# Kernel optimization log

Hardware: AMD Instinct MI355X
Metric: run time of the kernel (lower is better)

## Reference

```python
import jax, jax.numpy as jnp
import numpy as np

LN_EPS = 1e-5

def _layer_norm(x, g, b):
    mu = jnp.mean(x, axis=-1, keepdims=True)
    var = jnp.mean(jnp.square(x - mu), axis=-1, keepdims=True)
    return g * (x - mu) * jax.lax.rsqrt(var + LN_EPS) + b

def setup_inputs() -> dict:
    key = jax.random.key(0)
    ks = jax.random.split(key, 12)
    N, E, D, V = 25000, 400000, 128, 16
    x = jax.random.normal(ks[0], (N, 3), dtype=jnp.float32)
    h = jax.random.normal(ks[1], (N, D), dtype=jnp.float32)
    edge_index = jax.random.randint(ks[2], (2, E), 0, N, dtype=jnp.int64)
    local_frames = jax.random.normal(ks[3], (N, 3, 3), dtype=jnp.float32)
    batch = jnp.zeros((N,), dtype=jnp.int64)
    v_prev = jax.random.normal(ks[4], (N, V, 3), dtype=jnp.float32)
    # vector_init params: Linear(D, 3V) -> LN -> SiLU -> Linear(3V, 3V) -> LN -> SiLU
    lim1 = np.sqrt(6.0 / (D + 3 * V))
    W1 = jax.random.uniform(ks[5], (3 * V, D), minval=-lim1, maxval=lim1, dtype=jnp.float32)
    b1 = jnp.zeros((3 * V,), jnp.float32)
    g1 = jnp.ones((3 * V,), jnp.float32); bb1 = jnp.zeros((3 * V,), jnp.float32)
    lim2 = np.sqrt(6.0 / (3 * V + 3 * V))
    W2 = jax.random.uniform(ks[6], (3 * V, 3 * V), minval=-lim2, maxval=lim2, dtype=jnp.float32)
    b2 = jnp.zeros((3 * V,), jnp.float32)
    g2 = jnp.ones((3 * V,), jnp.float32); bb2 = jnp.zeros((3 * V,), jnp.float32)
    # vector_interaction params: Linear(2D, 2V*V) -> LN -> Sigmoid
    limi = np.sqrt(6.0 / (2 * D + 2 * V * V))
    Wi = jax.random.uniform(ks[7], (2 * V * V, 2 * D), minval=-limi, maxval=limi, dtype=jnp.float32)
    bi = jnp.zeros((2 * V * V,), jnp.float32)
    gi = jnp.ones((2 * V * V,), jnp.float32); bbi = jnp.zeros((2 * V * V,), jnp.float32)
    return {"x": x, "h": h, "edge_index": edge_index, "local_frames": local_frames,
            "batch": batch, "v_prev": v_prev,
            "W1": W1, "b1": b1, "g1": g1, "bb1": bb1,
            "W2": W2, "b2": b2, "g2": g2, "bb2": bb2,
            "Wi": Wi, "bi": bi, "gi": gi, "bbi": bbi}

def reference(x, h, edge_index, local_frames, batch, v_prev,
              W1, b1, g1, bb1, W2, b2, g2, bb2, Wi, bi, gi, bbi):
    N = x.shape[0]
    V = v_prev.shape[1]  # vector_dim
    row, col = edge_index[0], edge_index[1]
    # vector_init: two Linear+LN+SiLU blocks -> [N, V, 3]
    t = jax.nn.silu(_layer_norm(h @ W1.T + b1, g1, bb1))
    t = jax.nn.silu(_layer_norm(t @ W2.T + b2, g2, bb2))
    vectors = t.reshape(N, V, 3)
    hi, hj = h[col], h[row]           # [E, D]
    vi, vj = vectors[col], vectors[row]  # [E, V, 3]
    Ri, Rj = local_frames[col], local_frames[row]  # [E, 3, 3]
    # R_rel = Ri^T @ Rj
    R_rel = jnp.einsum('eji,ejk->eik', Ri, Rj)
    vj_in_i = jnp.einsum('eij,ecj->eci', R_rel, vj)  # rotate sender vectors
    stacked_vectors = jnp.concatenate([vi, vj_in_i], axis=1)  # [E, 2V, 3]
    stacked_norms = jnp.concatenate([hi, hj], axis=-1)        # [E, 2D]
    w = jax.nn.sigmoid(_layer_norm(stacked_norms @ Wi.T + bi, gi, bbi))
    int_weights = w.reshape(-1, 2 * V, V)                     # [E, 2V, V]
    v_new = jnp.einsum('eko,ekc->eco', stacked_vectors, int_weights)  # [E, V, 3]
    v_out = jax.ops.segment_sum(v_new, col, num_segments=N)  # scatter-add on receiver
    return v_prev + v_out
```

## Files before the change

kernel.cpp:

```cpp
#include <hip/hip_runtime.h>


#define DD 128
#define VV 16
#define TV 48
#define NK 512
#define LOG2E 1.44269504088896340736f

typedef __attribute__((ext_vector_type(8))) short short8;
typedef __attribute__((ext_vector_type(4))) float f32x4;

#if __has_builtin(__builtin_amdgcn_exp2f)
#define EXP2F(x) __builtin_amdgcn_exp2f(x)
#else
#define EXP2F(x) exp2f(x)
#endif
#if __has_builtin(__builtin_amdgcn_rcpf)
#define RCPF(x) __builtin_amdgcn_rcpf(x)
#else
#define RCPF(x) (1.0f/(x))
#endif

__device__ __forceinline__ unsigned short f2bf(float f){
    union{float f; unsigned u;} v; v.f = f;
    unsigned r = v.u + 0x7fffu + ((v.u >> 16) & 1u);
    return (unsigned short)(r >> 16);
}
__device__ __forceinline__ float bf2f(unsigned short h){
    union{unsigned u; float f;} v; v.u = ((unsigned)h) << 16; return v.f;
}
__device__ __forceinline__ float bf2f_hi(unsigned u){
    union{unsigned u; float f;} v; v.u = u & 0xffff0000u; return v.f;
}
__device__ __forceinline__ float bf2f_lo(unsigned u){
    union{unsigned u; float f;} v; v.u = u << 16; return v.f;
}
__device__ __forceinline__ void unpack8(uint4 q, float* d){
    d[0]=bf2f_lo(q.x); d[1]=bf2f_hi(q.x);
    d[2]=bf2f_lo(q.y); d[3]=bf2f_hi(q.y);
    d[4]=bf2f_lo(q.z); d[5]=bf2f_hi(q.z);
    d[6]=bf2f_lo(q.w); d[7]=bf2f_hi(q.w);
}
__device__ __forceinline__ float waveRedSum64(float v){
    #pragma unroll
    for (int off = 32; off > 0; off >>= 1) v += __shfl_xor(v, off, 64);
    return v;
}

__global__ void prep_k(const int* __restrict__ p, int nchk, int* __restrict__ flag,
                       int* __restrict__ cnt, int N){
    int i = blockIdx.x*blockDim.x + threadIdx.x;
    if (i < N) cnt[i] = 0;
    if (blockIdx.x == 0){
        __shared__ int s;
        if (threadIdx.x == 0) s = 0;
        __syncthreads();
        int nz = 0;
        for (int k = threadIdx.x; k < nchk; k += blockDim.x) nz |= (p[2*k+1] != 0);
        if (nz) atomicOr(&s, 1);
        __syncthreads();
        if (threadIdx.x == 0) *flag = s ? 0 : 1;
    }
}

__global__ void cvt_hist(const void* __restrict__ src, int* __restrict__ dst,
                         int* __restrict__ cnt, int n, int E,
                         const int* __restrict__ flag){
    int i = blockIdx.x*blockDim.x + threadIdx.x;
    if (i >= n) return;
    int v = (*flag) ? (int)((const long long*)src)[i] : ((const int*)src)[i];
    dst[i] = v;
    if (i >= E) atomicAdd(&cnt[v], 1);
}

__global__ __launch_bounds__(1024) void scan_k(const int* __restrict__ cnt,
        int* __restrict__ start, int* __restrict__ cursor, int N){
    __shared__ int wsum[16];
    __shared__ int woff[16];
    __shared__ int btot;
    __shared__ int carry;
    int tid = threadIdx.x;
    int lane = tid & 63, wid = tid >> 6;
    if (tid == 0) carry = 0;
    __syncthreads();
    for (int base = 0; base < N; base += 1024){
        int i = base + tid;
        int x = (i < N) ? cnt[i] : 0;
        int v = x;
        #pragma unroll
        for (int off = 1; off < 64; off <<= 1){
            int t = __shfl_up(v, off, 64);
            if (lane >= off) v += t;
        }
        if (lane == 63) wsum[wid] = v;
        __syncthreads();
        if (wid == 0 && lane < 16){
            int s = wsum[lane];
            int sv = s;
            #pragma unroll
            for (int off = 1; off < 16; off <<= 1){
                int t = __shfl_up(sv, off, 64);
                if (lane >= off) sv += t;
            }
            woff[lane] = sv - s;
            if (lane == 15) btot = sv;
        }
        __syncthreads();
        if (i < N){
            int excl = v - x + woff[wid] + carry;
            start[i] = excl;
            cursor[i] = excl;
        }
        __syncthreads();
        if (tid == 0) carry += btot;
        __syncthreads();
    }
    if (tid == 0) start[N] = carry;
}

__global__ void scatter_k(const int* __restrict__ idx, int* __restrict__ cursor,
                          int* __restrict__ elist, int E){
    int e = blockIdx.x*blockDim.x + threadIdx.x;
    if (e >= E) return;
    int col = idx[E + e], row = idx[e];
    int pos = atomicAdd(&cursor[col], 1);
    elist[pos] = row;
}

__global__ void build_wt(const float* __restrict__ Wi, const float* __restrict__ bi,
                         const float* __restrict__ gi, const float* __restrict__ bbi,
                         unsigned short* __restrict__ Wtb, float* __restrict__ bias_t,
                         float* __restrict__ gi_t, float* __restrict__ bbi_t){
    int j = blockIdx.x;
    int d = threadIdx.x;
    int half = j >> 9;
    int jj = j & 511;
    int c = jj >> 5, kk = jj & 31;
    int k = kk*16 + c;
    Wtb[(size_t)j*128 + d] = f2bf(Wi[k*256 + half*128 + d]);
    if (d == 0){
        bias_t[j] = half ? 0.0f : bi[k];
        if (!half){ gi_t[jj] = -gi[k]*LOG2E; bbi_t[jj] = -bbi[k]*LOG2E; }
    }
}

__global__ __launch_bounds__(256) void vinit(
        const float* __restrict__ h,
        const float* __restrict__ W1, const float* __restrict__ b1,
        const float* __restrict__ g1, const float* __restrict__ bb1,
        const float* __restrict__ W2, const float* __restrict__ b2,
        const float* __restrict__ g2, const float* __restrict__ bb2,
        const float* __restrict__ frames,
        float* __restrict__ vecs, float* __restrict__ gvec,
        unsigned short* __restrict__ hbh, unsigned short* __restrict__ hbl, int N){
    __shared__ float hs[4][DD];
    __shared__ float ts[4][TV];
    int w = threadIdx.x >> 6, l = threadIdx.x & 63;
    int n = blockIdx.x*4 + w;
    int nr = n < N ? n : N-1;
    float hv0 = h[(size_t)nr*DD + l];
    float hv1 = h[(size_t)nr*DD + 64 + l];
    hs[w][l]      = hv0;
    hs[w][l + 64] = hv1;
    if (n < N){
        unsigned short h0 = f2bf(hv0), h1 = f2bf(hv1);
        hbh[(size_t)n*DD + l]      = h0;
        hbh[(size_t)n*DD + 64 + l] = h1;
        hbl[(size_t)n*DD + l]      = f2bf(hv0 - bf2f(h0));
        hbl[(size_t)n*DD + 64 + l] = f2bf(hv1 - bf2f(h1));
    }
    __syncthreads();

    float o1 = 0.0f;
    if (l < TV){
        o1 = b1[l];
        const float* wr = W1 + l*DD;
        #pragma unroll
        for (int d = 0; d < DD; d += 4){
            float4 w4 = *(const float4*)(wr + d);
            o1 += hs[w][d]*w4.x + hs[w][d+1]*w4.y + hs[w][d+2]*w4.z + hs[w][d+3]*w4.w;
        }
    }
    float s  = waveRedSum64(l < TV ? o1 : 0.0f);
    float mu = s * (1.0f/TV);
    float dv = l < TV ? (o1 - mu) : 0.0f;
    float sq = waveRedSum64(dv*dv);
    float inv = rsqrtf(sq*(1.0f/TV) + 1e-5f);
    if (l < TV){
        float y = g1[l]*(dv*inv) + bb1[l];
        ts[w][l] = y / (1.0f + __expf(-y));
    }
    __syncthreads();

    float o2 = 0.0f;
    if (l < TV){
        o2 = b2[l];
        const float* wr = W2 + l*TV;
        #pragma unroll
        for (int j = 0; j < TV; j += 4){
            float4 w4 = *(const float4*)(wr + j);
            o2 += ts[w][j]*w4.x + ts[w][j+1]*w4.y + ts[w][j+2]*w4.z + ts[w][j+3]*w4.w;
        }
    }
    s  = waveRedSum64(l < TV ? o2 : 0.0f);
    mu = s * (1.0f/TV);
    dv = l < TV ? (o2 - mu) : 0.0f;
    sq = waveRedSum64(dv*dv);
    inv = rsqrtf(sq*(1.0f/TV) + 1e-5f);
    __syncthreads();
    if (l < TV){
        float y = g2[l]*(dv*inv) + bb2[l];
        float t2 = y / (1.0f + __expf(-y));
        if (n < N) vecs[(size_t)n*TV + l] = t2;
        ts[w][l] = t2;
    }
    __syncthreads();
    if (l < TV && n < N){
        int cc = l/3, oo = l%3;
        const float* R = frames + (size_t)n*9;
        float gv = R[oo*3+0]*ts[w][cc*3+0] + R[oo*3+1]*ts[w][cc*3+1] + R[oo*3+2]*ts[w][cc*3+2];
        gvec[(size_t)n*TV + l] = gv;
    }
}

__global__ __launch_bounds__(256) void gemm_mfma(
        const unsigned short* __restrict__ hbh, const unsigned short* __restrict__ hbl,
        const unsigned short* __restrict__ Wtb, const float* __restrict__ bias_t,
        unsigned short* __restrict__ P, int Np){
    int wv = threadIdx.x >> 6, l = threadIdx.x & 63;
    int lr = l & 15, g = l >> 4;
    int m0 = (blockIdx.y*4 + wv)*16;
    int n0 = blockIdx.x*256;

    f32x4 acc[16];
    #pragma unroll
    for (int nf = 0; nf < 16; nf++) acc[nf] = (f32x4){0.f,0.f,0.f,0.f};

    const unsigned short* arow_h = hbh + (size_t)(m0 + lr)*128;
    const unsigned short* arow_l = hbl + (size_t)(m0 + lr)*128;

    #pragma unroll
    for (int ks = 0; ks < 128; ks += 32){
        int kb = ks + 4*g;
        short8 ah, al;
        ((ushort4*)&ah)[0] = *(const ushort4*)(arow_h + kb);
        ((ushort4*)&ah)[1] = *(const ushort4*)(arow_h + kb + 16);
        ((ushort4*)&al)[0] = *(const ushort4*)(arow_l + kb);
        ((ushort4*)&al)[1] = *(const ushort4*)(arow_l + kb + 16);
        #pragma unroll
        for (int nf = 0; nf < 16; nf++){
            const unsigned short* brow = Wtb + (size_t)(n0 + nf*16 + lr)*128;
            short8 b;
            ((ushort4*)&b)[0] = *(const ushort4*)(brow + kb);
            ((ushort4*)&b)[1] = *(const ushort4*)(brow + kb + 16);
            acc[nf] = __builtin_amdgcn_mfma_f32_16x16x32_bf16(ah, b, acc[nf], 0, 0, 0);
            acc[nf] = __builtin_amdgcn_mfma_f32_16x16x32_bf16(al, b, acc[nf], 0, 0, 0);
        }
    }
    #pragma unroll
    for (int nf = 0; nf < 16; nf++){
        int col = n0 + nf*16 + lr;
        float bs = bias_t[col];
        #pragma unroll
        for (int r = 0; r < 4; r++){
            P[(size_t)(m0 + g*4 + r)*1024 + col] = f2bf(acc[nf][r] + bs);
        }
    }
}

__global__ __launch_bounds__(256) void node_k(
        const unsigned short* __restrict__ P, const float* __restrict__ vecs,
        const float* __restrict__ gvec, const float* __restrict__ frames,
        const int* __restrict__ start, const int* __restrict__ elist,
        const float* __restrict__ vprev, const float* __restrict__ gi_t,
        const float* __restrict__ bbi_t, float* __restrict__ out, int N){
    __shared__ float svs[4][4][100];
    int wv = threadIdx.x >> 6, ln = threadIdx.x & 63;
    int sub = ln >> 4, c = ln & 15;
    int n0 = blockIdx.x*4 + wv;
    int n = n0 < N ? n0 : N-1;

    {
        const float* vc = vecs + (size_t)n*TV + c*3;
        svs[wv][sub][c*3+0] = vc[0];
        svs[wv][sub][c*3+1] = vc[1];
        svs[wv][sub][c*3+2] = vc[2];
    }
    float R[9];
    #pragma unroll
    for (int i = 0; i < 9; i++) R[i] = frames[(size_t)n*9 + i];

    float pa[32];
    {
        const uint4* p4 = (const uint4*)(P + (size_t)n*1024 + c*32);
        #pragma unroll
        for (int q = 0; q < 4; q++) unpack8(p4[q], pa + 8*q);
    }
    int e0 = start[n], e1 = start[n+1];
    float a0 = 0.f, a1 = 0.f, a2 = 0.f;

    int t = e0 + sub;
    int rcur = elist[t < e1 ? t : 0];
    uint4 pb0, pb1, pb2, pb3;
    float gv0, gv1, gv2;
    {
        const uint4* p4 = (const uint4*)(P + (size_t)rcur*1024 + 512 + c*32);
        pb0 = p4[0]; pb1 = p4[1]; pb2 = p4[2]; pb3 = p4[3];
        const float* gr = gvec + (size_t)rcur*TV + c*3;
        gv0 = gr[0]; gv1 = gr[1]; gv2 = gr[2];
    }

    for (; t < e1; t += 4){
        int tn = t + 4;
        int rnext = elist[tn < e1 ? tn : 0];
        uint4 nb0, nb1, nb2, nb3;
        float ng0, ng1, ng2;
        {
            const uint4* p4 = (const uint4*)(P + (size_t)rnext*1024 + 512 + c*32);
            nb0 = p4[0]; nb1 = p4[1]; nb2 = p4[2]; nb3 = p4[3];
            const float* gr = gvec + (size_t)rnext*TV + c*3;
            ng0 = gr[0]; ng1 = gr[1]; ng2 = gr[2];
        }

        float l[32];
        unpack8(pb0, l+0); unpack8(pb1, l+8); unpack8(pb2, l+16); unpack8(pb3, l+24);
        float sA = 0.f, sB = 0.f, qA = 0.f, qB = 0.f;
        #pragma unroll
        for (int i = 0; i < 16; i++){
            float xa = pa[i]    + l[i];    l[i]    = xa; sA += xa; qA = fmaf(xa, xa, qA);
            float xb = pa[16+i] + l[16+i]; l[16+i] = xb; sB += xb; qB = fmaf(xb, xb, qB);
        }
        float s = sA + sB, sq = qA + qB;
        #pragma unroll
        for (int off = 1; off < 16; off <<= 1){
            s  += __shfl_xor(s,  off, 64);
            sq += __shfl_xor(sq, off, 64);
        }
        float mu  = s * (1.0f/NK);
        float var = fmaf(-mu, mu, sq * (1.0f/NK));
        float inv = rsqrtf(var + 1e-5f);
        float nmi = -mu * inv;

        svs[wv][sub][48+c*3+0] = R[0]*gv0 + R[3]*gv1 + R[6]*gv2;
        svs[wv][sub][48+c*3+1] = R[1]*gv0 + R[4]*gv1 + R[7]*gv2;
        svs[wv][sub][48+c*3+2] = R[2]*gv0 + R[5]*gv1 + R[8]*gv2;

        {
            const float4* g4 = (const float4*)(gi_t  + c*32);
            const float4* b4 = (const float4*)(bbi_t + c*32);
            #pragma unroll
            for (int q = 0; q < 8; q++){
                float4 gg = g4[q], bb = b4[q];
                float gx[4] = {gg.x, gg.y, gg.z, gg.w};
                float bx[4] = {bb.x, bb.y, bb.z, bb.w};
                #pragma unroll
                for (int r = 0; r < 4; r++){
                    float z   = fmaf(l[4*q+r], inv, nmi);
                    float arg = fmaf(gx[r], z, bx[r]);
                    l[4*q+r]  = RCPF(1.0f + EXP2F(arg));
                }
            }
        }
        {
            const float4* sv4 = (const float4*)&svs[wv][sub][0];
            #pragma unroll
            for (int q = 0; q < 24; q++){
                float4 x = sv4[q];
                {   const int e = 4*q+0, ch = e/3, o = e%3;
                    float p = x.x * l[ch];
                    if (o==0) a0 += p; else if (o==1) a1 += p; else a2 += p; }
                {   const int e = 4*q+1, ch = e/3, o = e%3;
                    float p = x.y * l[ch];
                    if (o==0) a0 += p; else if (o==1) a1 += p; else a2 += p; }
                {   const int e = 4*q+2, ch = e/3, o = e%3;
                    float p = x.z * l[ch];
                    if (o==0) a0 += p; else if (o==1) a1 += p; else a2 += p; }
                {   const int e = 4*q+3, ch = e/3, o = e%3;
                    float p = x.w * l[ch];
                    if (o==0) a0 += p; else if (o==1) a1 += p; else a2 += p; }
            }
        }
        pb0 = nb0; pb1 = nb1; pb2 = nb2; pb3 = nb3;
        gv0 = ng0; gv1 = ng1; gv2 = ng2;
    }
    a0 += __shfl_xor(a0,16,64); a0 += __shfl_xor(a0,32,64);
    a1 += __shfl_xor(a1,16,64); a1 += __shfl_xor(a1,32,64);
    a2 += __shfl_xor(a2,16,64); a2 += __shfl_xor(a2,32,64);
    if (ln < 16 && n0 < N){
        size_t o = (size_t)n*TV + c*3;
        out[o+0] = vprev[o+0] + a0;
        out[o+1] = vprev[o+1] + a1;
        out[o+2] = vprev[o+2] + a2;
    }
}

extern "C" void kernel_launch(void* const* d_in, const int* in_sizes, int n_in,
                              void* d_out, int out_size, void* d_ws, size_t ws_size,
                              hipStream_t stream){
    const float* h      = (const float*)d_in[1];
    const void*  eidx   = d_in[2];
    const float* frames = (const float*)d_in[3];
    const float* vprev  = (const float*)d_in[5];
    const float* W1  = (const float*)d_in[6];
    const float* b1  = (const float*)d_in[7];
    const float* g1  = (const float*)d_in[8];
    const float* bb1 = (const float*)d_in[9];
    const float* W2  = (const float*)d_in[10];
    const float* b2  = (const float*)d_in[11];
    const float* g2  = (const float*)d_in[12];
    const float* bb2 = (const float*)d_in[13];
    const float* Wi  = (const float*)d_in[14];
    const float* bi  = (const float*)d_in[15];
    const float* gi  = (const float*)d_in[16];
    const float* bbi = (const float*)d_in[17];
    float* out = (float*)d_out;

    const int N = in_sizes[1] / DD;
    const int E = in_sizes[2] / 2;
    const int Np = ((N + 63) / 64) * 64;

    float* bias_t = (float*)d_ws;
    float* gi_t   = bias_t + 1024;
    float* bbi_t  = gi_t + 512;
    float* vecs   = bbi_t + 512;
    float* gvec   = vecs + (size_t)N*TV;
    unsigned short* Wtb = (unsigned short*)(gvec + (size_t)N*TV);
    unsigned short* hbh = Wtb + 1024*128;
    unsigned short* hbl = hbh + (size_t)Np*128;
    unsigned short* P   = hbl + (size_t)Np*128;
    int* idx32  = (int*)(P + (size_t)Np*1024);
    int* cnt    = idx32 + 2*(size_t)E;
    int* startp = cnt + N;
    int* cursor = startp + N + 1;
    int* elist  = cursor + N;
    int* dflag  = elist + E;

    int nchk = E < 4096 ? E : 4096;
    prep_k<<<(N + 255)/256, 256, 0, stream>>>((const int*)eidx, nchk, dflag, cnt, N);
    cvt_hist<<<(2*E + 255)/256, 256, 0, stream>>>(eidx, idx32, cnt, 2*E, E, dflag);
    build_wt<<<1024, 128, 0, stream>>>(Wi, bi, gi, bbi, Wtb, bias_t, gi_t, bbi_t);
    vinit<<<(N + 3)/4, 256, 0, stream>>>(h, W1, b1, g1, bb1, W2, b2, g2, bb2,
                                         frames, vecs, gvec, hbh, hbl, N);
    gemm_mfma<<<dim3(4, Np/64), 256, 0, stream>>>(hbh, hbl, Wtb, bias_t, P, Np);
    scan_k<<<1, 1024, 0, stream>>>(cnt, startp, cursor, N);
    scatter_k<<<(E + 255)/256, 256, 0, stream>>>(idx32, cursor, elist, E);
    node_k<<<(N + 3)/4, 256, 0, stream>>>(P, vecs, gvec, frames, startp, elist,
                                          vprev, gi_t, bbi_t, out, N);
    (void)ws_size; (void)n_in; (void)out_size;
}
```

Measured before the change: 582.1 us.

## Replace single-block prefix scan with three-phase multi-block scan

```diff
diff --git a/kernel.cpp b/kernel.cpp
--- a/kernel.cpp
+++ b/kernel.cpp
@@ -73,49 +73,64 @@
     if (i >= E) atomicAdd(&cnt[v], 1);
 }
 
-__global__ __launch_bounds__(1024) void scan_k(const int* __restrict__ cnt,
-        int* __restrict__ start, int* __restrict__ cursor, int N){
+__global__ __launch_bounds__(256) void scan_blk(const int* __restrict__ cnt,
+        int* __restrict__ start, int* __restrict__ bsum, int N){
+    __shared__ int wsum[4];
+    int tid = threadIdx.x, lane = tid & 63, wid = tid >> 6;
+    int i = blockIdx.x*256 + tid;
+    int x = (i < N) ? cnt[i] : 0;
+    int v = x;
+    #pragma unroll
+    for (int off = 1; off < 64; off <<= 1){
+        int t = __shfl_up(v, off, 64);
+        if (lane >= off) v += t;
+    }
+    if (lane == 63) wsum[wid] = v;
+    __syncthreads();
+    int woff = 0;
+    #pragma unroll
+    for (int k = 0; k < 4; k++) woff += (k < wid) ? wsum[k] : 0;
+    if (i < N) start[i] = v - x + woff;
+    if (tid == 255) bsum[blockIdx.x] = woff + v;
+}
+
+__global__ __launch_bounds__(1024) void scan_top(const int* __restrict__ bsum,
+        int* __restrict__ boff, int* __restrict__ start, int NB, int N){
     __shared__ int wsum[16];
     __shared__ int woff[16];
-    __shared__ int btot;
-    __shared__ int carry;
-    int tid = threadIdx.x;
-    int lane = tid & 63, wid = tid >> 6;
-    if (tid == 0) carry = 0;
-    __syncthreads();
-    for (int base = 0; base < N; base += 1024){
-        int i = base + tid;
-        int x = (i < N) ? cnt[i] : 0;
-        int v = x;
-        #pragma unroll
-        for (int off = 1; off < 64; off <<= 1){
-            int t = __shfl_up(v, off, 64);
-            if (lane >= off) v += t;
-        }
-        if (lane == 63) wsum[wid] = v;
-        __syncthreads();
-        if (wid == 0 && lane < 16){
-            int s = wsum[lane];
-            int sv = s;
-            #pragma unroll
-            for (int off = 1; off < 16; off <<= 1){
-                int t = __shfl_up(sv, off, 64);
-                if (lane >= off) sv += t;
-            }
-            woff[lane] = sv - s;
-            if (lane == 15) btot = sv;
-        }
-        __syncthreads();
-        if (i < N){
-            int excl = v - x + woff[wid] + carry;
-            start[i] = excl;
-            cursor[i] = excl;
-        }
-        __syncthreads();
-        if (tid == 0) carry += btot;
-        __syncthreads();
-    }
-    if (tid == 0) start[N] = carry;
+    int tid = threadIdx.x, lane = tid & 63, wid = tid >> 6;
+    int x = (tid < NB) ? bsum[tid] : 0;
+    int v = x;
+    #pragma unroll
+    for (int off = 1; off < 64; off <<= 1){
+        int t = __shfl_up(v, off, 64);
+        if (lane >= off) v += t;
+    }
+    if (lane == 63) wsum[wid] = v;
+    __syncthreads();
+    if (wid == 0 && lane < 16){
+        int s = wsum[lane];
+        int sv = s;
+        #pragma unroll
+        for (int off = 1; off < 16; off <<= 1){
+            int t = __shfl_up(sv, off, 64);
+            if (lane >= off) sv += t;
+        }
+        woff[lane] = sv - s;
+    }
+    __syncthreads();
+    if (tid < NB) boff[tid] = v - x + woff[wid];
+    if (tid == 1023) start[N] = woff[15] + v;
+}
+
+__global__ void scan_add(int* __restrict__ start, int* __restrict__ cursor,
+                         const int* __restrict__ boff, int N){
+    int i = blockIdx.x*blockDim.x + threadIdx.x;
+    if (i < N){
+        int s = start[i] + boff[i >> 8];
+        start[i] = s;
+        cursor[i] = s;
+    }
 }
 
 __global__ void scatter_k(const int* __restrict__ idx, int* __restrict__ cursor,
@@ -418,6 +433,7 @@
     const int N = in_sizes[1] / DD;
     const int E = in_sizes[2] / 2;
     const int Np = ((N + 63) / 64) * 64;
+    const int NB = (N + 255) / 256;
 
     float* bias_t = (float*)d_ws;
     float* gi_t   = bias_t + 1024;
@@ -434,6 +450,8 @@
     int* cursor = startp + N + 1;
     int* elist  = cursor + N;
     int* dflag  = elist + E;
+    int* bsum   = dflag + 1;
+    int* boff   = bsum + 1024;
 
     int nchk = E < 4096 ? E : 4096;
     prep_k<<<(N + 255)/256, 256, 0, stream>>>((const int*)eidx, nchk, dflag, cnt, N);
@@ -442,7 +460,9 @@
     vinit<<<(N + 3)/4, 256, 0, stream>>>(h, W1, b1, g1, bb1, W2, b2, g2, bb2,
                                          frames, vecs, gvec, hbh, hbl, N);
     gemm_mfma<<<dim3(4, Np/64), 256, 0, stream>>>(hbh, hbl, Wtb, bias_t, P, Np);
-    scan_k<<<1, 1024, 0, stream>>>(cnt, startp, cursor, N);
+    scan_blk<<<NB, 256, 0, stream>>>(cnt, startp, bsum, N);
+    scan_top<<<1, 1024, 0, stream>>>(bsum, boff, startp, NB, N);
+    scan_add<<<NB, 256, 0, stream>>>(startp, cursor, boff, N);
     scatter_k<<<(E + 255)/256, 256, 0, stream>>>(idx32, cursor, elist, E);
     node_k<<<(N + 3)/4, 256, 0, stream>>>(P, vecs, gvec, frames, startp, elist,
                                           vprev, gi_t, bbi_t, out, N);
```

After: 564.0 us. 3.1% less time.
